# Kernel optimization log

Hardware: AMD Instinct MI355X
Metric: run time of the kernel (lower is better)

Reference implementation:

```python
import jax, jax.numpy as jnp
import numpy as np

S = 4096      # keystrokes
H = 32        # hidden_dim / d_model
NH = 8        # nhead
HD = H // NH  # head dim = 4
FF = 2048     # torch TransformerEncoderLayer default dim_feedforward
NL = 6        # num_layers
EPS = 1e-5


def setup_inputs() -> dict:
    key = jax.random.key(0)
    ks = jax.random.split(key, 20)
    sc = 0.02
    ts = jnp.sort(jax.random.uniform(ks[0], (S,), minval=0.0, maxval=2.49e7))
    feats = jax.random.normal(ks[1], (S, 2), dtype=jnp.float32)
    data = jnp.concatenate([ts[:, None], feats], axis=1)  # [S, 3]
    return {
        "data": data,
        "lin_w": jax.random.normal(ks[2], (H, 2)) * sc,
        "lin_b": jnp.zeros((H,)),
        "qkv_w": jax.random.normal(ks[3], (NL, 3 * H, H)) * sc,
        "qkv_b": jnp.zeros((NL, 3 * H)),
        "out_w": jax.random.normal(ks[4], (NL, H, H)) * sc,
        "out_b": jnp.zeros((NL, H)),
        "ln1_g": jnp.ones((NL, H)),
        "ln1_b": jnp.zeros((NL, H)),
        "ff1_w": jax.random.normal(ks[5], (NL, FF, H)) * sc,
        "ff1_b": jnp.zeros((NL, FF)),
        "ff2_w": jax.random.normal(ks[6], (NL, H, FF)) * sc,
        "ff2_b": jnp.zeros((NL, H)),
        "ln2_g": jnp.ones((NL, H)),
        "ln2_b": jnp.zeros((NL, H)),
        "cls_w": jax.random.normal(ks[7], (1, H)) * sc,
        "cls_b": jnp.zeros((1,)),
    }


def _ln(x, g, b):
    m = x.mean(-1, keepdims=True)
    v = ((x - m) ** 2).mean(-1, keepdims=True)
    return (x - m) / jnp.sqrt(v + EPS) * g + b


def reference(data, lin_w, lin_b, qkv_w, qkv_b, out_w, out_b,
              ln1_g, ln1_b, ff1_w, ff1_b, ff2_w, ff2_b,
              ln2_g, ln2_b, cls_w, cls_b):
    # per-keystroke Linear+ReLU, vectorized over the sequence
    x = jax.nn.relu(data[:, 1:] @ lin_w.T + lin_b)            # [S, H]
    # sinusoidal time encoding at index timestamp//100
    ts_idx = (data[:, 0] / 100.0).astype(jnp.int32)            # [S]
    div = jnp.exp(jnp.arange(0, H, 2, dtype=jnp.float32) * (-np.log(10000.0) / H))
    ang = ts_idx[:, None].astype(jnp.float32) * div            # [S, H/2]
    pe = jnp.stack([jnp.sin(ang), jnp.cos(ang)], axis=-1).reshape(S, H)
    x = x + pe
    # prepend CLS token of -1.0 -> seq len S+1
    x = jnp.concatenate([jnp.full((1, H), -1.0, dtype=x.dtype), x], axis=0)
    L = S + 1
    for i in range(NL):  # post-LN encoder layers (torch defaults, eval/no-dropout)
        qkv = x @ qkv_w[i].T + qkv_b[i]                        # [L, 3H]
        q, k, v = jnp.split(qkv, 3, axis=-1)
        q = q.reshape(L, NH, HD)
        k = k.reshape(L, NH, HD)
        v = v.reshape(L, NH, HD)
        scores = jnp.einsum('qhd,khd->hqk', q, k) / np.sqrt(HD)
        attn = jax.nn.softmax(scores, axis=-1)                 # [NH, L, L]
        o = jnp.einsum('hqk,khd->qhd', attn, v).reshape(L, H)
        o = o @ out_w[i].T + out_b[i]
        x = _ln(x + o, ln1_g[i], ln1_b[i])
        f = jax.nn.relu(x @ ff1_w[i].T + ff1_b[i]) @ ff2_w[i].T + ff2_b[i]
        x = _ln(x + f, ln2_g[i], ln2_b[i])
    cls_out = x[0]                                             # [H]
    return jax.nn.sigmoid(cls_out @ cls_w.T + cls_b)           # [1]
```

## Files before the change

### kernel.cpp

```cpp
#include <hip/hip_runtime.h>
#include <hip/hip_bf16.h>
#include <math.h>

#define SEQ 4096
#define LL  4097
#define HDIM 32
#define FFD 2048
#define NLAYER 6
#define EPSLN 1e-5f
#define NCHUNK 16
#define KPAD 4128
#define QROWS 4352
#define RB2 16

#if __has_builtin(__builtin_amdgcn_exp2f)
#define EXP2 __builtin_amdgcn_exp2f
#else
#define EXP2 exp2f
#endif

#define QSCALE 0.7213475204444817f

typedef short bf16x8 __attribute__((ext_vector_type(8)));
typedef short bf16x4 __attribute__((ext_vector_type(4)));
typedef float f32x4 __attribute__((ext_vector_type(4)));

__device__ __forceinline__ unsigned short f2b(float f) {
  unsigned int b = __float_as_uint(f);
  b += 0x7FFFu + ((b >> 16) & 1u);
  return (unsigned short)(b >> 16);
}

__device__ __forceinline__ float b2f(unsigned short u) {
  unsigned int b = ((unsigned int)u) << 16;
  return __uint_as_float(b);
}

__device__ __forceinline__ unsigned int pk_bf16(float a, float b) {
  __hip_bfloat162 h = __float22bfloat162_rn(make_float2(a, b));
  return *(unsigned int*)&h;
}

__device__ __forceinline__ f32x4 mfma_qk(bf16x4 a, bf16x4 b, f32x4 c) {
#if __has_builtin(__builtin_amdgcn_mfma_f32_16x16x16bf16_1k)
  return __builtin_amdgcn_mfma_f32_16x16x16bf16_1k(a, b, c, 0, 0, 0);
#else
  bf16x8 a8 = {a[0], a[1], a[2], a[3], 0, 0, 0, 0};
  bf16x8 b8 = {b[0], b[1], b[2], b[3], 0, 0, 0, 0};
  return __builtin_amdgcn_mfma_f32_16x16x32_bf16(a8, b8, c, 0, 0, 0);
#endif
}


__device__ __forceinline__ void qkv_wave(float y, int row, bool ok, int lane,
    const float* __restrict__ qw, const float* __restrict__ qb,
    unsigned short* __restrict__ Qb, unsigned short* __restrict__ KB4,
    unsigned short* __restrict__ VB5) {
  int ch = lane & 31;
  float xv[32];
#pragma unroll
  for (int k = 0; k < 32; ++k) xv[k] = __shfl(y, (lane & 32) + k, 64);
#pragma unroll
  for (int t3 = 0; t3 < 3; ++t3) {
    int cc = t3 * 32 + ch;
    const float4* wr = (const float4*)(qw + (size_t)cc * 32);
    float acc = qb[cc];
#pragma unroll
    for (int k8 = 0; k8 < 8; ++k8) {
      float4 wv = wr[k8];
      acc = fmaf(xv[4 * k8 + 0], wv.x, acc);
      acc = fmaf(xv[4 * k8 + 1], wv.y, acc);
      acc = fmaf(xv[4 * k8 + 2], wv.z, acc);
      acc = fmaf(xv[4 * k8 + 3], wv.w, acc);
    }
    if (ok) {
      int h = ch >> 2;
      if (t3 == 0) {
        Qb[(size_t)row * 32 + ch] = f2b(QSCALE * acc);
      } else if (t3 == 1) {
        KB4[((size_t)h * KPAD + row) * 4 + (ch & 3)] = f2b(acc);
      } else {
        int w = row & 31;
        int pos = ((w & 15) << 1) | (w >> 4);
        VB5[((size_t)h * 5 + (ch & 3)) * KPAD + (row & ~31) + pos] = f2b(acc);
      }
    }
  }
}

__global__ __launch_bounds__(256) void k_init(const float* __restrict__ data,
    const float* __restrict__ lin_w, const float* __restrict__ lin_b,
    const float* __restrict__ qkv_w, const float* __restrict__ qkv_b,
    const float* __restrict__ ff1_w, const float* __restrict__ ff2_w,
    float* __restrict__ X, unsigned short* __restrict__ Qb,
    unsigned short* __restrict__ KB4, unsigned short* __restrict__ VB5,
    unsigned short* __restrict__ W1B, unsigned short* __restrict__ W2B) {
  int gid = blockIdx.x * 256 + threadIdx.x;
  int gsz = gridDim.x * 256;
  const int NW = NLAYER * FFD * 32;
  for (int i = gid; i < NW; i += gsz) {
    W1B[i] = f2b(ff1_w[i]);
    W2B[i] = f2b(ff2_w[i]);
  }
  for (int i = gid; i < (QROWS - LL) * 32; i += gsz)
    Qb[(size_t)LL * 32 + i] = 0;
  for (int i = gid; i < 8 * (KPAD - LL) * 4; i += gsz) {
    int hh = i / ((KPAD - LL) * 4);
    int rem = i % ((KPAD - LL) * 4);
    KB4[((size_t)hh * KPAD + LL) * 4 + rem] = 0;
  }
  for (int i = gid; i < 8 * 5 * KPAD; i += gsz) {
    int col = i % KPAD;
    int dd = (i / KPAD) % 5;
    if (dd == 4) {
      int key = (col & ~31) + ((col & 1) << 4) + ((col & 31) >> 1);
      VB5[i] = (key <= 4096) ? 0x3F80 : 0;
    } else if (col > 4096) {
      VB5[i] = 0;
    }
  }
  int wave = threadIdx.x >> 6, lane = threadIdx.x & 63;
  int r = lane >> 5, ch = lane & 31;
  unsigned wgid = blockIdx.x * 4 + wave;
  for (unsigned it = wgid; it < 2049; it += gridDim.x * 4) {
    int row = it * 2 + r;
    bool ok = row < LL;
    float val = 0.f;
    if (ok) {
      if (row == 0) {
        val = -1.0f;
      } else {
        int s = row - 1;
        float ts = data[s * 3 + 0];
        float f0 = data[s * 3 + 1];
        float f1 = data[s * 3 + 2];
        float lin = f0 * lin_w[ch * 2 + 0] + f1 * lin_w[ch * 2 + 1] + lin_b[ch];
        lin = fmaxf(lin, 0.0f);
        int tsi = (int)(ts / 100.0f);
        int j = ch >> 1;
        float aj = (float)(2 * j) * (float)(-0.28782313662425575);
        float divj = (float)exp((double)aj);
        float ang = (float)tsi * divj;
        float pe = (ch & 1) ? cosf(ang) : sinf(ang);
        val = lin + pe;
      }
      X[(size_t)row * HDIM + ch] = val;
    }
    qkv_wave(val, row, ok, lane, qkv_w, qkv_b, Qb, KB4, VB5);
  }
}

__global__ __launch_bounds__(256, 4) void k_attn(
    const unsigned short* __restrict__ Qb, const unsigned short* __restrict__ KB4,
    const unsigned short* __restrict__ VB5, float* __restrict__ LP,
    float4* __restrict__ AP4) {
  int tid = threadIdx.x;
  int wave = tid >> 6, lane = tid & 63;
  int l16 = lane & 15, quad = lane >> 4;
  int h = blockIdx.y, c = blockIdx.z;
  int qs = blockIdx.x * 4 + wave;
  if (qs >= 65) return;
  int q0 = qs * 64;
  int kb0 = c * 256;
  int nkb = (c == NCHUNK - 1) ? 9 : 8;

  const unsigned short* KBh = KB4 + (size_t)h * KPAD * 4;
  const unsigned short* VBh = VB5 + (size_t)h * 5 * KPAD;
  const bool kl = (quad == (h & 3));
  const bool vl = (l16 < 5);
  const int qcol0 = (h >> 2) * 16 + quad * 4;

  bf16x4 aq[4];
#pragma unroll
  for (int t = 0; t < 4; ++t)
    aq[t] = *(const bf16x4*)&Qb[(size_t)(q0 + t * 16 + l16) * 32 + qcol0];

  const bf16x4 zb4 = {0, 0, 0, 0};
  const bf16x8 zb8 = {0, 0, 0, 0, 0, 0, 0, 0};
  f32x4 acc0[4], acc1[4];
#pragma unroll
  for (int t = 0; t < 4; ++t) {
    acc0[t] = (f32x4){0.f, 0.f, 0.f, 0.f};
    acc1[t] = (f32x4){0.f, 0.f, 0.f, 0.f};
  }

  auto step = [&](int k0, f32x4* acc) {
    bf16x4 bk0 = kl ? *(const bf16x4*)&KBh[(size_t)(k0 + l16) * 4] : zb4;
    bf16x4 bk1 = kl ? *(const bf16x4*)&KBh[(size_t)(k0 + 16 + l16) * 4] : zb4;
    bf16x8 bv = vl ? *(const bf16x8*)&VBh[(size_t)l16 * KPAD + k0 + quad * 8]
                   : zb8;
    f32x4 z = {0.f, 0.f, 0.f, 0.f};
    unsigned pf[4][4];
#pragma unroll
    for (int t = 0; t < 4; ++t) {
      f32x4 s0 = mfma_qk(bk0, aq[t], z);
      f32x4 s1 = mfma_qk(bk1, aq[t], z);
#pragma unroll
      for (int reg = 0; reg < 4; ++reg)
        pf[t][reg] = pk_bf16(EXP2(s0[reg]), EXP2(s1[reg]));
    }
#pragma unroll
    for (int t = 0; t < 4; ++t) {
      bf16x8 pb = *(const bf16x8*)&pf[t][0];
      acc[t] = __builtin_amdgcn_mfma_f32_16x16x32_bf16(bv, pb, acc[t], 0, 0, 0);
    }
  };

  int kb = 0;
  for (; kb + 2 <= nkb; kb += 2) {
    step(kb0 + kb * 32, acc0);
    step(kb0 + (kb + 1) * 32, acc1);
  }
  if (kb < nkb) step(kb0 + kb * 32, acc0);

#pragma unroll
  for (int t = 0; t < 4; ++t) {
    f32x4 a = acc0[t] + acc1[t];
    int q = q0 + t * 16 + l16;
    if (q < LL) {
      if (quad == 0) {
        AP4[((size_t)c * LL + q) * 8 + h] = make_float4(a[0], a[1], a[2], a[3]);
      } else if (quad == 1) {
        LP[((size_t)c * LL + q) * 8 + h] = a[0];
      }
    }
  }
}

__global__ __launch_bounds__(512, 4) void k_ffnF(const float* __restrict__ LP,
    const float* __restrict__ APf, float* __restrict__ X,
    const float* __restrict__ ow, const float* __restrict__ ob,
    const float* __restrict__ g1, const float* __restrict__ b1ln,
    const unsigned short* __restrict__ w1b, const float* __restrict__ fb1,
    const unsigned short* __restrict__ w2b, const float* __restrict__ fb2,
    const float* __restrict__ g2, const float* __restrict__ b2ln,
    const float* __restrict__ qw, const float* __restrict__ qb,
    unsigned short* __restrict__ Qb, unsigned short* __restrict__ KB4,
    unsigned short* __restrict__ VB5) {
  __shared__ unsigned short Xa[RB2][32];
  __shared__ float Y1[RB2][32];
  __shared__ unsigned short Fsb[8][16 * 136];
  __shared__ float Pr[8][RB2 * 33];
  int tid = threadIdx.x;
  int wave = tid >> 6, lane = tid & 63;
  int l16 = lane & 15, quad = lane >> 4;
  int r = lane >> 5, ch = lane & 31;
  int r0 = blockIdx.x * RB2;

  {
    int rl = wave * 2 + r;
    int row = r0 + rl;
    bool ok = row < LL;
    int hh = ch >> 2;
    float L = 0.f, A = 0.f;
    if (ok) {
#pragma unroll
      for (int c = 0; c < NCHUNK; ++c) {
        A += APf[((size_t)c * LL + row) * 32 + ch];
        L += LP[((size_t)c * LL + row) * 8 + hh];
      }
    }
    float os = ok ? A / L : 0.f;
    float acc = 0.f;
    const float4* owr = (const float4*)(ow + (size_t)ch * 32);
#pragma unroll
    for (int k8 = 0; k8 < 8; ++k8) {
      float4 wv = owr[k8];
      acc = fmaf(__shfl(os, (lane & 32) + 4 * k8 + 0, 64), wv.x, acc);
      acc = fmaf(__shfl(os, (lane & 32) + 4 * k8 + 1, 64), wv.y, acc);
      acc = fmaf(__shfl(os, (lane & 32) + 4 * k8 + 2, 64), wv.z, acc);
      acc = fmaf(__shfl(os, (lane & 32) + 4 * k8 + 3, 64), wv.w, acc);
    }
    float val = ok ? (X[(size_t)row * HDIM + ch] + acc + ob[ch]) : 0.f;
    float mean = val;
#pragma unroll
    for (int off = 16; off > 0; off >>= 1) mean += __shfl_xor(mean, off, 32);
    mean *= (1.f / 32.f);
    float d2 = val - mean;
    float var = d2 * d2;
#pragma unroll
    for (int off = 16; off > 0; off >>= 1) var += __shfl_xor(var, off, 32);
    var *= (1.f / 32.f);
    float y = d2 / sqrtf(var + EPSLN) * g1[ch] + b1ln[ch];
    Y1[rl][ch] = y;
    Xa[rl][ch] = ok ? f2b(y) : 0;
  }
  __syncthreads();

  bf16x8 a1 = *(const bf16x8*)&Xa[l16][quad * 8];
  f32x4 acc2[2] = {{0.f, 0.f, 0.f, 0.f}, {0.f, 0.f, 0.f, 0.f}};
  int fs0 = wave * 256;
#pragma unroll
  for (int sg = 0; sg < 2; ++sg) {
    int f0 = fs0 + sg * 128;
    f32x4 c1[8];
#pragma unroll
    for (int t = 0; t < 8; ++t) {
      bf16x8 b =
          *(const bf16x8*)&w1b[(size_t)(f0 + t * 16 + l16) * 32 + quad * 8];
      f32x4 z = {0.f, 0.f, 0.f, 0.f};
      c1[t] = __builtin_amdgcn_mfma_f32_16x16x32_bf16(a1, b, z, 0, 0, 0);
    }
#pragma unroll
    for (int t = 0; t < 8; ++t) {
      float bb = fb1[f0 + t * 16 + l16];
#pragma unroll
      for (int reg = 0; reg < 4; ++reg) {
        float v = fmaxf(c1[t][reg] + bb, 0.f);
        Fsb[wave][(quad * 4 + reg) * 136 + t * 16 + l16] = f2b(v);
      }
    }
#pragma unroll
    for (int kt = 0; kt < 4; ++kt) {
      bf16x8 a2 = *(const bf16x8*)&Fsb[wave][l16 * 136 + kt * 32 + quad * 8];
#pragma unroll
      for (int u = 0; u < 2; ++u) {
        bf16x8 b = *(const bf16x8*)&w2b[(size_t)(u * 16 + l16) * FFD + f0 +
                                        kt * 32 + quad * 8];
        acc2[u] =
            __builtin_amdgcn_mfma_f32_16x16x32_bf16(a2, b, acc2[u], 0, 0, 0);
      }
    }
  }
#pragma unroll
  for (int u = 0; u < 2; ++u)
#pragma unroll
    for (int reg = 0; reg < 4; ++reg)
      Pr[wave][(quad * 4 + reg) * 33 + u * 16 + l16] = acc2[u][reg];
  __syncthreads();

  {
    int rl = wave * 2 + r;
    int row = r0 + rl;
    bool ok = row < LL;
    float s = 0.f;
#pragma unroll
    for (int w = 0; w < 8; ++w) s += Pr[w][rl * 33 + ch];
    float val = ok ? (Y1[rl][ch] + s + fb2[ch]) : 0.f;
    float mean = val;
#pragma unroll
    for (int off = 16; off > 0; off >>= 1) mean += __shfl_xor(mean, off, 32);
    mean *= (1.f / 32.f);
    float d2 = val - mean;
    float var = d2 * d2;
#pragma unroll
    for (int off = 16; off > 0; off >>= 1) var += __shfl_xor(var, off, 32);
    var *= (1.f / 32.f);
    float y = d2 / sqrtf(var + EPSLN) * g2[ch] + b2ln[ch];
    if (ok) X[(size_t)row * HDIM + ch] = y;
    qkv_wave(y, row, ok, lane, qw, qb, Qb, KB4, VB5);
  }
}

__global__ __launch_bounds__(256) void k_last(
    const unsigned short* __restrict__ Qb, const unsigned short* __restrict__ KB4,
    const unsigned short* __restrict__ VB5, const float* __restrict__ X,
    const float* __restrict__ ow, const float* __restrict__ ob,
    const float* __restrict__ g1, const float* __restrict__ b1ln,
    const float* __restrict__ w1, const float* __restrict__ fb1,
    const float* __restrict__ w2, const float* __restrict__ fb2,
    const float* __restrict__ g2, const float* __restrict__ b2ln,
    const float* __restrict__ cw, const float* __restrict__ cb,
    float* __restrict__ out) {
  __shared__ float os_sh[32];
  __shared__ float y1_sh[32];
  __shared__ float f_sh[FFD];
  __shared__ float red[8][32];
  int tid = threadIdx.x;
  int h = tid >> 5, l32 = tid & 31;

  float q[4];
#pragma unroll
  for (int d = 0; d < 4; ++d) q[d] = b2f(Qb[h * 4 + d]);
  float num[4] = {0.f, 0.f, 0.f, 0.f};
  float den = 0.f;
#pragma unroll 2
  for (int k = l32; k < LL; k += 32) {
    bf16x4 kr = *(const bf16x4*)&KB4[((size_t)h * KPAD + k) * 4];
    float s = 0.f;
#pragma unroll
    for (int d = 0; d < 4; ++d)
      s = fmaf(q[d], b2f((unsigned short)kr[d]), s);
    float p = EXP2(s);
    int w = k & 31;
    int pos = (k & ~31) + (((w & 15) << 1) | (w >> 4));
#pragma unroll
    for (int d = 0; d < 4; ++d)
      num[d] = fmaf(p, b2f(VB5[((size_t)h * 5 + d) * KPAD + pos]), num[d]);
    den += p;
  }
#pragma unroll
  for (int off = 16; off > 0; off >>= 1) {
#pragma unroll
    for (int d = 0; d < 4; ++d) num[d] += __shfl_xor(num[d], off, 32);
    den += __shfl_xor(den, off, 32);
  }
  if (l32 < 4) os_sh[h * 4 + l32] = num[l32] / den;
  __syncthreads();

  if (tid < 32) {
    int ch = tid;
    float acc = 0.f;
#pragma unroll
    for (int k = 0; k < 32; ++k) acc = fmaf(os_sh[k], ow[ch * 32 + k], acc);
    float val = X[ch] + acc + ob[ch];
    float mean = val;
#pragma unroll
    for (int off = 16; off > 0; off >>= 1) mean += __shfl_xor(mean, off, 32);
    mean *= (1.f / 32.f);
    float d2 = val - mean;
    float var = d2 * d2;
#pragma unroll
    for (int off = 16; off > 0; off >>= 1) var += __shfl_xor(var, off, 32);
    var *= (1.f / 32.f);
    y1_sh[ch] = d2 / sqrtf(var + EPSLN) * g1[ch] + b1ln[ch];
  }
  __syncthreads();

  for (int i = tid; i < FFD; i += 256) {
    const float* wr = w1 + (size_t)i * 32;
    float acc = fb1[i];
#pragma unroll
    for (int j = 0; j < 32; ++j) acc = fmaf(y1_sh[j], wr[j], acc);
    f_sh[i] = fmaxf(acc, 0.f);
  }
  __syncthreads();

  {
    float acc = 0.f;
    const float* wr = w2 + (size_t)l32 * FFD + h * 256;
    const float* fr = &f_sh[h * 256];
#pragma unroll 8
    for (int j = 0; j < 256; ++j) acc = fmaf(fr[j], wr[j], acc);
    red[h][l32] = acc;
  }
  __syncthreads();

  if (tid < 32) {
    int ch = tid;
    float s = 0.f;
#pragma unroll
    for (int sg = 0; sg < 8; ++sg) s += red[sg][ch];
    float val = y1_sh[ch] + s + fb2[ch];
    float mean = val;
#pragma unroll
    for (int off = 16; off > 0; off >>= 1) mean += __shfl_xor(mean, off, 32);
    mean *= (1.f / 32.f);
    float d2 = val - mean;
    float var = d2 * d2;
#pragma unroll
    for (int off = 16; off > 0; off >>= 1) var += __shfl_xor(var, off, 32);
    var *= (1.f / 32.f);
    float y = d2 / sqrtf(var + EPSLN) * g2[ch] + b2ln[ch];
    float t = y * cw[ch];
#pragma unroll
    for (int off = 16; off > 0; off >>= 1) t += __shfl_xor(t, off, 32);
    if (ch == 0) out[0] = 1.f / (1.f + expf(-(t + cb[0])));
  }
}

extern "C" void kernel_launch(void* const* d_in, const int* in_sizes, int n_in,
                              void* d_out, int out_size, void* d_ws,
                              size_t ws_size, hipStream_t stream) {
  const float* data  = (const float*)d_in[0];
  const float* lin_w = (const float*)d_in[1];
  const float* lin_b = (const float*)d_in[2];
  const float* qkv_w = (const float*)d_in[3];
  const float* qkv_b = (const float*)d_in[4];
  const float* out_w = (const float*)d_in[5];
  const float* out_b = (const float*)d_in[6];
  const float* ln1_g = (const float*)d_in[7];
  const float* ln1_b = (const float*)d_in[8];
  const float* ff1_w = (const float*)d_in[9];
  const float* ff1_b = (const float*)d_in[10];
  const float* ff2_w = (const float*)d_in[11];
  const float* ff2_b = (const float*)d_in[12];
  const float* ln2_g = (const float*)d_in[13];
  const float* ln2_b = (const float*)d_in[14];
  const float* cls_w = (const float*)d_in[15];
  const float* cls_b = (const float*)d_in[16];

  char* wsb = (char*)d_ws;
  float* X = (float*)wsb;
  unsigned short* Qb  = (unsigned short*)(X + (size_t)LL * 32);
  unsigned short* KB4 = Qb + (size_t)QROWS * 32;
  unsigned short* VB5 = KB4 + (size_t)8 * KPAD * 4;
  unsigned short* W1B = VB5 + (size_t)8 * 5 * KPAD;
  unsigned short* W2B = W1B + (size_t)NLAYER * FFD * 32;
  float4* AP = (float4*)(((size_t)(W2B + (size_t)NLAYER * FFD * 32) + 15) &
                         ~(size_t)15);
  float* LP = (float*)(AP + (size_t)NCHUNK * LL * 8);

  k_init<<<1024, 256, 0, stream>>>(data, lin_w, lin_b, qkv_w, qkv_b,
                                   ff1_w, ff2_w, X, Qb, KB4, VB5, W1B, W2B);
  for (int l = 0; l < NLAYER - 1; ++l) {
    k_attn<<<dim3(17, 8, NCHUNK), 256, 0, stream>>>(Qb, KB4, VB5, LP, AP);
    const float* qw = qkv_w + (size_t)(l + 1) * 96 * 32;
    const float* qb = qkv_b + (size_t)(l + 1) * 96;
    k_ffnF<<<(LL + RB2 - 1) / RB2, 512, 0, stream>>>(
        LP, (const float*)AP, X,
        out_w + (size_t)l * 32 * 32, out_b + (size_t)l * 32,
        ln1_g + (size_t)l * 32, ln1_b + (size_t)l * 32,
        W1B + (size_t)l * FFD * 32, ff1_b + (size_t)l * FFD,
        W2B + (size_t)l * FFD * 32, ff2_b + (size_t)l * 32,
        ln2_g + (size_t)l * 32, ln2_b + (size_t)l * 32,
        qw, qb, Qb, KB4, VB5);
  }
  {
    const int l = NLAYER - 1;
    k_last<<<1, 256, 0, stream>>>(
        Qb, KB4, VB5, X,
        out_w + (size_t)l * 32 * 32, out_b + (size_t)l * 32,
        ln1_g + (size_t)l * 32, ln1_b + (size_t)l * 32,
        ff1_w + (size_t)l * FFD * 32, ff1_b + (size_t)l * FFD,
        ff2_w + (size_t)l * 32 * FFD, ff2_b + (size_t)l * 32,
        ln2_g + (size_t)l * 32, ln2_b + (size_t)l * 32,
        cls_w, cls_b, (float*)d_out);
  }
}
```

Measured before the change: 405.2 us.

## Parallelize final-layer CLS path across blocks using chunked attention and split FFN

The last layer's single-block kernel, which ran attention over all keys and the whole FFN serially, is replaced. Attention for the CLS row now reuses the chunked k_attn kernel on one query tile, and the FFN is split across 32 blocks that each write partial sums, followed by a tiny reduction kernel for LN2 and the classifier. It also switches the FFN weights to the pre-converted bf16 copies. The aim is to remove a long serial tail on one CU, at the cost of two extra kernel launches and some redundant LN1 work per block.

```diff
diff --git a/kernel.cpp b/kernel.cpp
--- a/kernel.cpp
+++ b/kernel.cpp
@@ -12,6 +12,7 @@
 #define KPAD 4128
 #define QROWS 4352
 #define RB2 16
+#define LB 32
 
 #if __has_builtin(__builtin_amdgcn_exp2f)
 #define EXP2 __builtin_amdgcn_exp2f
@@ -352,57 +353,32 @@
   }
 }
 
-__global__ __launch_bounds__(256) void k_last(
-    const unsigned short* __restrict__ Qb, const unsigned short* __restrict__ KB4,
-    const unsigned short* __restrict__ VB5, const float* __restrict__ X,
+__global__ __launch_bounds__(256) void k_lastB(const float* __restrict__ LP,
+    const float* __restrict__ APf, const float* __restrict__ X,
     const float* __restrict__ ow, const float* __restrict__ ob,
     const float* __restrict__ g1, const float* __restrict__ b1ln,
-    const float* __restrict__ w1, const float* __restrict__ fb1,
-    const float* __restrict__ w2, const float* __restrict__ fb2,
-    const float* __restrict__ g2, const float* __restrict__ b2ln,
-    const float* __restrict__ cw, const float* __restrict__ cb,
-    float* __restrict__ out) {
-  __shared__ float os_sh[32];
+    const unsigned short* __restrict__ w1b, const float* __restrict__ fb1,
+    const unsigned short* __restrict__ w2b, float* __restrict__ y1_ws,
+    float* __restrict__ part) {
   __shared__ float y1_sh[32];
-  __shared__ float f_sh[FFD];
+  __shared__ float f_sh[64];
   __shared__ float red[8][32];
   int tid = threadIdx.x;
-  int h = tid >> 5, l32 = tid & 31;
-
-  float q[4];
-#pragma unroll
-  for (int d = 0; d < 4; ++d) q[d] = b2f(Qb[h * 4 + d]);
-  float num[4] = {0.f, 0.f, 0.f, 0.f};
-  float den = 0.f;
-#pragma unroll 2
-  for (int k = l32; k < LL; k += 32) {
-    bf16x4 kr = *(const bf16x4*)&KB4[((size_t)h * KPAD + k) * 4];
-    float s = 0.f;
-#pragma unroll
-    for (int d = 0; d < 4; ++d)
-      s = fmaf(q[d], b2f((unsigned short)kr[d]), s);
-    float p = EXP2(s);
-    int w = k & 31;
-    int pos = (k & ~31) + (((w & 15) << 1) | (w >> 4));
-#pragma unroll
-    for (int d = 0; d < 4; ++d)
-      num[d] = fmaf(p, b2f(VB5[((size_t)h * 5 + d) * KPAD + pos]), num[d]);
-    den += p;
-  }
-#pragma unroll
-  for (int off = 16; off > 0; off >>= 1) {
-#pragma unroll
-    for (int d = 0; d < 4; ++d) num[d] += __shfl_xor(num[d], off, 32);
-    den += __shfl_xor(den, off, 32);
-  }
-  if (l32 < 4) os_sh[h * 4 + l32] = num[l32] / den;
-  __syncthreads();
+  int b = blockIdx.x;
 
   if (tid < 32) {
-    int ch = tid;
+    int ch = tid, hh = ch >> 2;
+    float A = 0.f, L = 0.f;
+#pragma unroll
+    for (int c = 0; c < NCHUNK; ++c) {
+      A += APf[((size_t)c * LL) * 32 + ch];
+      L += LP[((size_t)c * LL) * 8 + hh];
+    }
+    float os = A / L;
     float acc = 0.f;
 #pragma unroll
-    for (int k = 0; k < 32; ++k) acc = fmaf(os_sh[k], ow[ch * 32 + k], acc);
+    for (int k = 0; k < 32; ++k)
+      acc = fmaf(__shfl(os, k, 32), ow[ch * 32 + k], acc);
     float val = X[ch] + acc + ob[ch];
     float mean = val;
 #pragma unroll
@@ -413,50 +389,65 @@
 #pragma unroll
     for (int off = 16; off > 0; off >>= 1) var += __shfl_xor(var, off, 32);
     var *= (1.f / 32.f);
-    y1_sh[ch] = d2 / sqrtf(var + EPSLN) * g1[ch] + b1ln[ch];
+    float y = d2 / sqrtf(var + EPSLN) * g1[ch] + b1ln[ch];
+    y1_sh[ch] = y;
+    if (b == 0) y1_ws[ch] = y;
   }
   __syncthreads();
 
-  for (int i = tid; i < FFD; i += 256) {
-    const float* wr = w1 + (size_t)i * 32;
+  if (tid < 64) {
+    int i = b * 64 + tid;
+    const unsigned short* wr = w1b + (size_t)i * 32;
     float acc = fb1[i];
 #pragma unroll
-    for (int j = 0; j < 32; ++j) acc = fmaf(y1_sh[j], wr[j], acc);
-    f_sh[i] = fmaxf(acc, 0.f);
+    for (int j = 0; j < 32; ++j) acc = fmaf(y1_sh[j], b2f(wr[j]), acc);
+    f_sh[tid] = fmaxf(acc, 0.f);
   }
   __syncthreads();
 
   {
+    int ch = tid & 31, seg = tid >> 5;
     float acc = 0.f;
-    const float* wr = w2 + (size_t)l32 * FFD + h * 256;
-    const float* fr = &f_sh[h * 256];
-#pragma unroll 8
-    for (int j = 0; j < 256; ++j) acc = fmaf(fr[j], wr[j], acc);
-    red[h][l32] = acc;
+    const unsigned short* wr = w2b + (size_t)ch * FFD + b * 64 + seg * 8;
+#pragma unroll
+    for (int j = 0; j < 8; ++j) acc = fmaf(f_sh[seg * 8 + j], b2f(wr[j]), acc);
+    red[seg][ch] = acc;
   }
   __syncthreads();
-
   if (tid < 32) {
-    int ch = tid;
     float s = 0.f;
 #pragma unroll
-    for (int sg = 0; sg < 8; ++sg) s += red[sg][ch];
-    float val = y1_sh[ch] + s + fb2[ch];
-    float mean = val;
-#pragma unroll
-    for (int off = 16; off > 0; off >>= 1) mean += __shfl_xor(mean, off, 32);
-    mean *= (1.f / 32.f);
-    float d2 = val - mean;
-    float var = d2 * d2;
-#pragma unroll
-    for (int off = 16; off > 0; off >>= 1) var += __shfl_xor(var, off, 32);
-    var *= (1.f / 32.f);
-    float y = d2 / sqrtf(var + EPSLN) * g2[ch] + b2ln[ch];
-    float t = y * cw[ch];
-#pragma unroll
-    for (int off = 16; off > 0; off >>= 1) t += __shfl_xor(t, off, 32);
-    if (ch == 0) out[0] = 1.f / (1.f + expf(-(t + cb[0])));
-  }
+    for (int sg = 0; sg < 8; ++sg) s += red[sg][tid];
+    part[b * 32 + tid] = s;
+  }
+}
+
+__global__ __launch_bounds__(64) void k_lastC(const float* __restrict__ y1_ws,
+    const float* __restrict__ part, const float* __restrict__ fb2,
+    const float* __restrict__ g2, const float* __restrict__ b2ln,
+    const float* __restrict__ cw, const float* __restrict__ cb,
+    float* __restrict__ out) {
+  int tid = threadIdx.x;
+  if (tid >= 32) return;
+  int ch = tid;
+  float s = 0.f;
+#pragma unroll 4
+  for (int b = 0; b < LB; ++b) s += part[b * 32 + ch];
+  float val = y1_ws[ch] + s + fb2[ch];
+  float mean = val;
+#pragma unroll
+  for (int off = 16; off > 0; off >>= 1) mean += __shfl_xor(mean, off, 32);
+  mean *= (1.f / 32.f);
+  float d2 = val - mean;
+  float var = d2 * d2;
+#pragma unroll
+  for (int off = 16; off > 0; off >>= 1) var += __shfl_xor(var, off, 32);
+  var *= (1.f / 32.f);
+  float y = d2 / sqrtf(var + EPSLN) * g2[ch] + b2ln[ch];
+  float t = y * cw[ch];
+#pragma unroll
+  for (int off = 16; off > 0; off >>= 1) t += __shfl_xor(t, off, 32);
+  if (ch == 0) out[0] = 1.f / (1.f + expf(-(t + cb[0])));
 }
 
 extern "C" void kernel_launch(void* const* d_in, const int* in_sizes, int n_in,
@@ -490,6 +481,8 @@
   float4* AP = (float4*)(((size_t)(W2B + (size_t)NLAYER * FFD * 32) + 15) &
                          ~(size_t)15);
   float* LP = (float*)(AP + (size_t)NCHUNK * LL * 8);
+  float* Y1W = LP + (size_t)NCHUNK * LL * 8;
+  float* PART = Y1W + 32;
 
   k_init<<<1024, 256, 0, stream>>>(data, lin_w, lin_b, qkv_w, qkv_b,
                                    ff1_w, ff2_w, X, Qb, KB4, VB5, W1B, W2B);
@@ -508,13 +501,16 @@
   }
   {
     const int l = NLAYER - 1;
-    k_last<<<1, 256, 0, stream>>>(
-        Qb, KB4, VB5, X,
+    k_attn<<<dim3(1, 8, NCHUNK), 256, 0, stream>>>(Qb, KB4, VB5, LP, AP);
+    k_lastB<<<LB, 256, 0, stream>>>(
+        LP, (const float*)AP, X,
         out_w + (size_t)l * 32 * 32, out_b + (size_t)l * 32,
         ln1_g + (size_t)l * 32, ln1_b + (size_t)l * 32,
-        ff1_w + (size_t)l * FFD * 32, ff1_b + (size_t)l * FFD,
-        ff2_w + (size_t)l * 32 * FFD, ff2_b + (size_t)l * 32,
-        ln2_g + (size_t)l * 32, ln2_b + (size_t)l * 32,
-        cls_w, cls_b, (float*)d_out);
-  }
-}
+        W1B + (size_t)l * FFD * 32, ff1_b + (size_t)l * FFD,
+        W2B + (size_t)l * FFD * 32, Y1W, PART);
+    k_lastC<<<1, 64, 0, stream>>>(Y1W, PART, ff2_b + (size_t)l * 32,
+                                  ln2_g + (size_t)l * 32,
+                                  ln2_b + (size_t)l * 32,
+                                  cls_w, cls_b, (float*)d_out);
+  }
+}
```

New measurement: 367.4 us (median of 2 runs). 9.3% less time.
